# Performance work log

Measured on AMD Instinct MI355X. Metric: run time of the kernel, lower is better.

## Reference

```python
import math
import jax, jax.numpy as jnp
import numpy as np

B, T, C, H = 4, 2048, 1024, 1024

def setup_inputs() -> dict:
    key = jax.random.key(0)
    kx, kk, kq, kv = jax.random.split(key, 4)
    s = 1.0 / math.sqrt(C)
    return {
        "x": jax.random.normal(kx, (B, T, C), dtype=jnp.float32),
        # torch Linear weight is [out, in]; store transposed [in, out] for x @ W
        "Wk": jax.random.uniform(kk, (C, H), dtype=jnp.float32, minval=-s, maxval=s),
        "Wq": jax.random.uniform(kq, (C, H), dtype=jnp.float32, minval=-s, maxval=s),
        "Wv": jax.random.uniform(kv, (C, H), dtype=jnp.float32, minval=-s, maxval=s),
    }

def reference(x, Wk, Wq, Wv):
    K = x @ Wk  # [B,T,H]
    Q = x @ Wq
    V = x @ Wv
    scale = 1.0 / math.sqrt(K.shape[-1])
    wei = jnp.einsum('bth,bsh->bts', Q, K) * scale  # [B,T,T]
    t = x.shape[1]
    causal = jnp.tril(jnp.ones((t, t), dtype=bool))
    wei = jnp.where(causal, wei, -jnp.inf)
    wei = jax.nn.softmax(wei, axis=-1)
    wei = jax.nn.relu(wei)  # no-op mathematically but kept for fidelity
    return jnp.einsum('bts,bsh->bth', wei, V)
```

## Files before the change

### kernel.cpp

```cpp
#include <hip/hip_runtime.h>

typedef _Float16 f16;
typedef _Float16 f16x8 __attribute__((ext_vector_type(8)));
typedef float    f32x4 __attribute__((ext_vector_type(4)));

#define AS3 __attribute__((address_space(3)))
#define AS1 __attribute__((address_space(1)))

static __device__ __forceinline__ void gld_lds16(const f16* g, f16* l) {
    __builtin_amdgcn_global_load_lds((const AS1 void*)g, (AS3 void*)l, 16, 0, 0);
}


__global__ void cvt_x(const float* __restrict__ x, f16* __restrict__ xh) {
    int i = blockIdx.x * blockDim.x + threadIdx.x;
    const f32x4* xv = (const f32x4*)x;
    f32x4 a = xv[2 * i], b = xv[2 * i + 1];
    f16x8 h;
    h[0] = (f16)a[0]; h[1] = (f16)a[1]; h[2] = (f16)a[2]; h[3] = (f16)a[3];
    h[4] = (f16)b[0]; h[5] = (f16)b[1]; h[6] = (f16)b[2]; h[7] = (f16)b[3];
    ((f16x8*)xh)[i] = h;
}

__global__ void cvt_transpose_w(const float* __restrict__ Wq, const float* __restrict__ Wk,
                                const float* __restrict__ Wv, f16* __restrict__ Wt) {
    const float* W = blockIdx.z == 0 ? Wq : (blockIdx.z == 1 ? Wk : Wv);
    __shared__ float tile[32][33];
    int tx = threadIdx.x, ty = threadIdx.y;
    int n0 = blockIdx.x * 32, k0 = blockIdx.y * 32;
#pragma unroll
    for (int r = 0; r < 4; ++r)
        tile[ty + r * 8][tx] = W[(size_t)(k0 + ty + r * 8) * 1024 + n0 + tx];
    __syncthreads();
    f16* o = Wt + (size_t)blockIdx.z * 1024 * 1024;
#pragma unroll
    for (int r = 0; r < 4; ++r)
        o[(size_t)(n0 + ty + r * 8) * 1024 + k0 + tx] = (f16)tile[tx][ty + r * 8];
}

template <int MODE>
__global__ __launch_bounds__(256, 4)
void gemm128(const f16* __restrict__ A, int lda, long aStride,
             const f16* __restrict__ B, int ldb, long bStride,
             void* __restrict__ Cout, int ldc, long cStride,
             int ktiles, float scale, float* __restrict__ lsum,
             const f16* __restrict__ A2, const f16* __restrict__ B2,
             void* __restrict__ C2) {
    int bm, bn, bz = blockIdx.z;
    int m0, n0;
    const f16 *Ab, *Bb;
    char* Cb;

    if (MODE == 0) {
        bn = blockIdx.x; bm = blockIdx.y;
        n0 = bn * 128;
        if (bm < 64) {
            m0 = bm * 128;
            Ab = A; Bb = B; Cb = (char*)Cout;
        } else {
            int t = bm - 64;
            int bb = t >> 3;
            m0 = (t & 7) * 128;
            Ab = A2;
            Bb = B2 + (long)bb * 2048 * 1024;
            Cb = (char*)C2 + (long)bb * 1024 * 2048 * sizeof(f16);
        }
    } else if (MODE == 1) {
        int i = blockIdx.x;
        float ff = sqrtf(8.f * (float)i + 1.f);
        bm = (int)((ff - 1.f) * 0.5f);
        while ((bm + 1) * (bm + 2) / 2 <= i) ++bm;
        while (bm * (bm + 1) / 2 > i) --bm;
        bn = i - bm * (bm + 1) / 2;
        m0 = bm * 128; n0 = bn * 128;
        Ab = A + (long)bz * aStride;
        Bb = B + (long)bz * bStride;
        Cb = (char*)Cout + (long)bz * cStride * sizeof(f16);
    } else {
        bn = blockIdx.x; bm = gridDim.y - 1 - blockIdx.y;
        int lim = 4 * (bm + 1); if (lim < ktiles) ktiles = lim;
        m0 = bm * 128; n0 = bn * 128;
        Ab = A + (long)bz * aStride;
        Bb = B + (long)bz * bStride;
        Cb = (char*)Cout + (long)bz * cStride * sizeof(float);
    }

    __shared__ f16 lds[2 * 8192];

    const int tid = threadIdx.x;
    const int wave = tid >> 6, lane = tid & 63;
    const int q = lane >> 4, rr = lane & 15;
    const int wm = (wave >> 1) * 64, wn = (wave & 1) * 64;

    const int kcs = (((tid & 3) - (lane >> 4)) & 3) * 8;
    const f16* pA = Ab + (long)(m0 + (tid >> 2)) * lda + kcs;
    const f16* pB = Bb + (long)(n0 + (tid >> 2)) * ldb + kcs;

    auto stage = [&](int kt, int buf) {
        const int k0 = kt * 32;
        f16* lA = lds + buf * 8192 + wave * 512;
        f16* lB = lds + buf * 8192 + 4096 + wave * 512;
#pragma unroll
        for (int it = 0; it < 2; ++it) {
            gld_lds16(pA + (long)it * 64 * lda + k0, lA + it * 2048);
            gld_lds16(pB + (long)it * 64 * ldb + k0, lB + it * 2048);
        }
    };

    const int slotf = ((q + (rr >> 2)) & 3) * 8;

    f32x4 acc[4][4] = {};

    stage(0, 0);
    __syncthreads();

    for (int kt = 0; kt < ktiles; ++kt) {
        const int cur = kt & 1;
        if (kt + 1 < ktiles) stage(kt + 1, 1 - cur);
        const f16* bufA = lds + cur * 8192;
        const f16* bufB = bufA + 4096;
        f16x8 af[4], bf[4];
#pragma unroll
        for (int i = 0; i < 4; ++i)
            af[i] = *(const f16x8*)&bufA[(wm + i * 16 + rr) * 32 + slotf];
#pragma unroll
        for (int j = 0; j < 4; ++j)
            bf[j] = *(const f16x8*)&bufB[(wn + j * 16 + rr) * 32 + slotf];
#pragma unroll
        for (int i = 0; i < 4; ++i)
#pragma unroll
            for (int j = 0; j < 4; ++j)
                acc[i][j] = __builtin_amdgcn_mfma_f32_16x16x32_f16(af[i], bf[j], acc[i][j], 0, 0, 0);
        __syncthreads();
    }

#pragma unroll
    for (int i = 0; i < 4; ++i) {
#pragma unroll
        for (int r2 = 0; r2 < 4; ++r2) {
            const int row = wm + i * 16 + q * 4 + r2;
            float psum = 0.f;
            float inv = 1.f;
            if (MODE == 2) inv = 1.0f / lsum[bz * 2048 + m0 + row];
#pragma unroll
            for (int j = 0; j < 4; ++j) {
                const int col = wn + j * 16 + rr;
                float v = acc[i][j][r2] * scale;
                long idx = (long)(m0 + row) * ldc + n0 + col;
                if (MODE == 1) {
                    v = __expf(v);
                    if (n0 + col > m0 + row) v = 0.f;
                    psum += v;
                    ((f16*)Cb)[idx] = (f16)v;
                } else if (MODE == 0) {
                    ((f16*)Cb)[idx] = (f16)v;
                } else {
                    ((float*)Cb)[idx] = v * inv;
                }
            }
            if (MODE == 1) {
                psum += __shfl_xor(psum, 1, 64);
                psum += __shfl_xor(psum, 2, 64);
                psum += __shfl_xor(psum, 4, 64);
                psum += __shfl_xor(psum, 8, 64);
                if (rr == 0) atomicAdd(&lsum[bz * 2048 + m0 + row], psum);
            }
        }
    }
}

extern "C" void kernel_launch(void* const* d_in, const int* in_sizes, int n_in,
                              void* d_out, int out_size, void* d_ws, size_t ws_size,
                              hipStream_t stream) {
    (void)in_sizes; (void)n_in; (void)out_size; (void)ws_size;
    const float* x  = (const float*)d_in[0];
    const float* Wk = (const float*)d_in[1];
    const float* Wq = (const float*)d_in[2];
    const float* Wv = (const float*)d_in[3];
    float* out = (float*)d_out;

    const long MB = 1l << 20;
    char* ws = (char*)d_ws;
    f16*   qk   = (f16*)(ws);
    f16*   Vt   = (f16*)(ws + 32 * MB);
    f16*   P    = (f16*)(ws + 48 * MB);
    float* lsum = (float*)(ws + 80 * MB);
    f16*   xh   = (f16*)(ws + 81 * MB);
    f16*   Wt   = (f16*)(ws + 97 * MB);

    cvt_x<<<4096, 256, 0, stream>>>(x, xh);
    cvt_transpose_w<<<dim3(32, 32, 3), dim3(32, 8), 0, stream>>>(Wq, Wk, Wv, Wt);
    hipMemsetAsync(lsum, 0, 4 * 2048 * sizeof(float), stream);

    gemm128<0><<<dim3(16, 96, 1), 256, 0, stream>>>(xh, 1024, 0, Wt, 1024, 0,
                                                    qk, 2048, 0, 32, 1.0f, nullptr,
                                                    Wt + 2l * 1024 * 1024, xh, Vt);
    gemm128<1><<<dim3(136, 1, 4), 256, 0, stream>>>(qk, 2048, 2048l * 2048,
                                                    qk + 1024, 2048, 2048l * 2048,
                                                    P, 2048, 2048l * 2048, 32, 0.03125f, lsum,
                                                    nullptr, nullptr, nullptr);
    gemm128<2><<<dim3(8, 16, 4), 256, 0, stream>>>(P, 2048, 2048l * 2048,
                                                   Vt, 2048, 1024l * 2048,
                                                   out, 1024, 2048l * 1024, 64, 1.0f, lsum,
                                                   nullptr, nullptr, nullptr);
}
```

Measured before the change: 246.4 us.

## Fuse conversion kernels, add 2-wave projection GEMM, widen epilogue stores

Merges the x conversion, weight transpose and lsum memset into one launch, which removes two launches and a memset. The projection GEMM becomes a new 128-thread kernel in which each wave computes a 128x64 tile, giving more register reuse per wave at lower occupancy. The epilogues of all GEMMs pair adjacent columns with a lane shuffle so each store writes 32 or 64 bits instead of 16 or 32. The risks are register pressure from the larger accumulator array and fewer waves available to hide latency.

```diff
diff --git a/kernel.cpp b/kernel.cpp
--- a/kernel.cpp
+++ b/kernel.cpp
@@ -11,31 +11,131 @@
     __builtin_amdgcn_global_load_lds((const AS1 void*)g, (AS3 void*)l, 16, 0, 0);
 }
 
-
-__global__ void cvt_x(const float* __restrict__ x, f16* __restrict__ xh) {
-    int i = blockIdx.x * blockDim.x + threadIdx.x;
-    const f32x4* xv = (const f32x4*)x;
-    f32x4 a = xv[2 * i], b = xv[2 * i + 1];
-    f16x8 h;
-    h[0] = (f16)a[0]; h[1] = (f16)a[1]; h[2] = (f16)a[2]; h[3] = (f16)a[3];
-    h[4] = (f16)b[0]; h[5] = (f16)b[1]; h[6] = (f16)b[2]; h[7] = (f16)b[3];
-    ((f16x8*)xh)[i] = h;
-}
-
-__global__ void cvt_transpose_w(const float* __restrict__ Wq, const float* __restrict__ Wk,
-                                const float* __restrict__ Wv, f16* __restrict__ Wt) {
-    const float* W = blockIdx.z == 0 ? Wq : (blockIdx.z == 1 ? Wk : Wv);
+static __device__ __forceinline__ unsigned pack_f16(float a, float b) {
+    union { f16 h[2]; unsigned u; } p;
+    p.h[0] = (f16)a; p.h[1] = (f16)b;
+    return p.u;
+}
+
+__global__ void cvt_fused(const float* __restrict__ x, f16* __restrict__ xh,
+                          const float* __restrict__ Wq, const float* __restrict__ Wk,
+                          const float* __restrict__ Wv, f16* __restrict__ Wt,
+                          float* __restrict__ lsum) {
     __shared__ float tile[32][33];
-    int tx = threadIdx.x, ty = threadIdx.y;
-    int n0 = blockIdx.x * 32, k0 = blockIdx.y * 32;
-#pragma unroll
-    for (int r = 0; r < 4; ++r)
-        tile[ty + r * 8][tx] = W[(size_t)(k0 + ty + r * 8) * 1024 + n0 + tx];
+    const int bid = blockIdx.x;
+    if (bid < 4096) {
+        int i = bid * 256 + threadIdx.x;
+        const f32x4* xv = (const f32x4*)x;
+        f32x4 a = xv[2 * i], b = xv[2 * i + 1];
+        f16x8 h;
+        h[0] = (f16)a[0]; h[1] = (f16)a[1]; h[2] = (f16)a[2]; h[3] = (f16)a[3];
+        h[4] = (f16)b[0]; h[5] = (f16)b[1]; h[6] = (f16)b[2]; h[7] = (f16)b[3];
+        ((f16x8*)xh)[i] = h;
+        if (bid == 0) {
+#pragma unroll
+            for (int k = 0; k < 32; ++k) lsum[threadIdx.x * 32 + k] = 0.f;
+        }
+    } else {
+        int b2 = bid - 4096;
+        int bx = b2 & 31, by = (b2 >> 5) & 31, bz = b2 >> 10;
+        const float* W = bz == 0 ? Wq : (bz == 1 ? Wk : Wv);
+        int tx = threadIdx.x & 31, ty = threadIdx.x >> 5;
+        int n0 = bx * 32, k0 = by * 32;
+#pragma unroll
+        for (int r = 0; r < 4; ++r)
+            tile[ty + r * 8][tx] = W[(size_t)(k0 + ty + r * 8) * 1024 + n0 + tx];
+        __syncthreads();
+        f16* o = Wt + (size_t)bz * 1024 * 1024;
+#pragma unroll
+        for (int r = 0; r < 4; ++r)
+            o[(size_t)(n0 + ty + r * 8) * 1024 + k0 + tx] = (f16)tile[tx][ty + r * 8];
+    }
+}
+
+__global__ __launch_bounds__(128, 2)
+void gemmw2(const f16* __restrict__ A, const f16* __restrict__ B, f16* __restrict__ C,
+            const f16* __restrict__ A2, const f16* __restrict__ B2, f16* __restrict__ C2) {
+    const int bn = blockIdx.x, bm = blockIdx.y;
+    const int n0 = bn * 128;
+    int m0; const f16 *Ab, *Bb; f16* Cb;
+    if (bm < 64) {
+        m0 = bm * 128; Ab = A; Bb = B; Cb = C;
+    } else {
+        int t = bm - 64, bb = t >> 3;
+        m0 = (t & 7) * 128;
+        Ab = A2;
+        Bb = B2 + (long)bb * 2048 * 1024;
+        Cb = C2 + (long)bb * 1024 * 2048;
+    }
+    const int lda = 1024, ldb = 1024, ldc = 2048, ktiles = 32;
+
+    __shared__ f16 lds[2 * 8192];
+
+    const int tid = threadIdx.x;
+    const int wave = tid >> 6, lane = tid & 63;
+    const int q = lane >> 4, rr = lane & 15;
+    const int wn = wave * 64;
+
+    const int kcs = (((lane & 3) - (lane >> 4)) & 3) * 8;
+    const f16* pA = Ab + (long)(m0 + (tid >> 2)) * lda + kcs;
+    const f16* pB = Bb + (long)(n0 + (tid >> 2)) * ldb + kcs;
+
+    auto stage = [&](int kt, int buf) {
+        const int k0 = kt * 32;
+        f16* base = lds + buf * 8192 + wave * 512;
+#pragma unroll
+        for (int it = 0; it < 4; ++it) {
+            gld_lds16(pA + (long)it * 32 * lda + k0, base + it * 1024);
+            gld_lds16(pB + (long)it * 32 * ldb + k0, base + 4096 + it * 1024);
+        }
+    };
+
+    const int slotf = ((q + (rr >> 2)) & 3) * 8;
+
+    f32x4 acc[8][4] = {};
+
+    stage(0, 0);
     __syncthreads();
-    f16* o = Wt + (size_t)blockIdx.z * 1024 * 1024;
-#pragma unroll
-    for (int r = 0; r < 4; ++r)
-        o[(size_t)(n0 + ty + r * 8) * 1024 + k0 + tx] = (f16)tile[tx][ty + r * 8];
+
+    for (int kt = 0; kt < ktiles; ++kt) {
+        const int cur = kt & 1;
+        if (kt + 1 < ktiles) stage(kt + 1, 1 - cur);
+        const f16* bufA = lds + cur * 8192;
+        const f16* bufB = bufA + 4096;
+        f16x8 bf[4];
+#pragma unroll
+        for (int j = 0; j < 4; ++j)
+            bf[j] = *(const f16x8*)&bufB[(wn + j * 16 + rr) * 32 + slotf];
+#pragma unroll
+        for (int ih = 0; ih < 2; ++ih) {
+            f16x8 af[4];
+#pragma unroll
+            for (int i = 0; i < 4; ++i)
+                af[i] = *(const f16x8*)&bufA[((ih * 4 + i) * 16 + rr) * 32 + slotf];
+#pragma unroll
+            for (int i = 0; i < 4; ++i)
+#pragma unroll
+                for (int j = 0; j < 4; ++j)
+                    acc[ih * 4 + i][j] =
+                        __builtin_amdgcn_mfma_f32_16x16x32_f16(af[i], bf[j], acc[ih * 4 + i][j], 0, 0, 0);
+        }
+        __syncthreads();
+    }
+
+#pragma unroll
+    for (int i = 0; i < 8; ++i)
+#pragma unroll
+        for (int r2 = 0; r2 < 4; ++r2) {
+            const int row = i * 16 + q * 4 + r2;
+#pragma unroll
+            for (int j = 0; j < 4; ++j) {
+                const int col = wn + j * 16 + rr;
+                float v = acc[i][j][r2];
+                float vo = __shfl_xor(v, 1, 64);
+                if ((rr & 1) == 0)
+                    *(unsigned*)(Cb + (long)(m0 + row) * ldc + n0 + col) = pack_f16(v, vo);
+            }
+        }
 }
 
 template <int MODE>
@@ -43,29 +143,13 @@
 void gemm128(const f16* __restrict__ A, int lda, long aStride,
              const f16* __restrict__ B, int ldb, long bStride,
              void* __restrict__ Cout, int ldc, long cStride,
-             int ktiles, float scale, float* __restrict__ lsum,
-             const f16* __restrict__ A2, const f16* __restrict__ B2,
-             void* __restrict__ C2) {
+             int ktiles, float scale, float* __restrict__ lsum) {
     int bm, bn, bz = blockIdx.z;
     int m0, n0;
     const f16 *Ab, *Bb;
     char* Cb;
 
-    if (MODE == 0) {
-        bn = blockIdx.x; bm = blockIdx.y;
-        n0 = bn * 128;
-        if (bm < 64) {
-            m0 = bm * 128;
-            Ab = A; Bb = B; Cb = (char*)Cout;
-        } else {
-            int t = bm - 64;
-            int bb = t >> 3;
-            m0 = (t & 7) * 128;
-            Ab = A2;
-            Bb = B2 + (long)bb * 2048 * 1024;
-            Cb = (char*)C2 + (long)bb * 1024 * 2048 * sizeof(f16);
-        }
-    } else if (MODE == 1) {
+    if (MODE == 1) {
         int i = blockIdx.x;
         float ff = sqrtf(8.f * (float)i + 1.f);
         bm = (int)((ff - 1.f) * 0.5f);
@@ -151,11 +235,14 @@
                     v = __expf(v);
                     if (n0 + col > m0 + row) v = 0.f;
                     psum += v;
-                    ((f16*)Cb)[idx] = (f16)v;
-                } else if (MODE == 0) {
-                    ((f16*)Cb)[idx] = (f16)v;
+                    float vo = __shfl_xor(v, 1, 64);
+                    if ((rr & 1) == 0)
+                        *(unsigned*)((f16*)Cb + idx) = pack_f16(v, vo);
                 } else {
-                    ((float*)Cb)[idx] = v * inv;
+                    v *= inv;
+                    float vo = __shfl_xor(v, 1, 64);
+                    if ((rr & 1) == 0)
+                        *(float2*)((float*)Cb + idx) = make_float2(v, vo);
                 }
             }
             if (MODE == 1) {
@@ -188,19 +275,14 @@
     f16*   xh   = (f16*)(ws + 81 * MB);
     f16*   Wt   = (f16*)(ws + 97 * MB);
 
-    cvt_x<<<4096, 256, 0, stream>>>(x, xh);
-    cvt_transpose_w<<<dim3(32, 32, 3), dim3(32, 8), 0, stream>>>(Wq, Wk, Wv, Wt);
-    hipMemsetAsync(lsum, 0, 4 * 2048 * sizeof(float), stream);
-
-    gemm128<0><<<dim3(16, 96, 1), 256, 0, stream>>>(xh, 1024, 0, Wt, 1024, 0,
-                                                    qk, 2048, 0, 32, 1.0f, nullptr,
-                                                    Wt + 2l * 1024 * 1024, xh, Vt);
+    cvt_fused<<<7168, 256, 0, stream>>>(x, xh, Wq, Wk, Wv, Wt, lsum);
+
+    gemmw2<<<dim3(16, 96), 128, 0, stream>>>(xh, Wt, qk,
+                                             Wt + 2l * 1024 * 1024, xh, Vt);
     gemm128<1><<<dim3(136, 1, 4), 256, 0, stream>>>(qk, 2048, 2048l * 2048,
                                                     qk + 1024, 2048, 2048l * 2048,
-                                                    P, 2048, 2048l * 2048, 32, 0.03125f, lsum,
-                                                    nullptr, nullptr, nullptr);
+                                                    P, 2048, 2048l * 2048, 32, 0.03125f, lsum);
     gemm128<2><<<dim3(8, 16, 4), 256, 0, stream>>>(P, 2048, 2048l * 2048,
                                                    Vt, 2048, 1024l * 2048,
-                                                   out, 1024, 2048l * 1024, 64, 1.0f, lsum,
-                                                   nullptr, nullptr, nullptr);
-}
+                                                   out, 1024, 2048l * 1024, 64, 1.0f, lsum);
+}
```

Result: slower. 255.9 us (+3.9%).

## Compute softmax row sums via MFMA in PV gemm, fuse convert kernels, pack stores

Applied to the files above, without the earlier changes.

Drops the atomicAdd row-sum reduction and the lsum memset. In the P·V gemm, waves with wn==0 accumulate row sums of P with an extra MFMA against a ones vector and share them through LDS. The two fp32->fp16 conversion kernels are merged into one launch. Epilogue stores are paired across lanes with a shuffle so each store writes two elements. The cost is extra MFMA work on half the waves, an extra barrier, and row sums taken from the fp16-rounded P values.

```diff
diff --git a/kernel.cpp b/kernel.cpp
--- a/kernel.cpp
+++ b/kernel.cpp
@@ -11,31 +11,40 @@
     __builtin_amdgcn_global_load_lds((const AS1 void*)g, (AS3 void*)l, 16, 0, 0);
 }
 
-
-__global__ void cvt_x(const float* __restrict__ x, f16* __restrict__ xh) {
-    int i = blockIdx.x * blockDim.x + threadIdx.x;
-    const f32x4* xv = (const f32x4*)x;
-    f32x4 a = xv[2 * i], b = xv[2 * i + 1];
-    f16x8 h;
-    h[0] = (f16)a[0]; h[1] = (f16)a[1]; h[2] = (f16)a[2]; h[3] = (f16)a[3];
-    h[4] = (f16)b[0]; h[5] = (f16)b[1]; h[6] = (f16)b[2]; h[7] = (f16)b[3];
-    ((f16x8*)xh)[i] = h;
-}
-
-__global__ void cvt_transpose_w(const float* __restrict__ Wq, const float* __restrict__ Wk,
-                                const float* __restrict__ Wv, f16* __restrict__ Wt) {
-    const float* W = blockIdx.z == 0 ? Wq : (blockIdx.z == 1 ? Wk : Wv);
+static __device__ __forceinline__ unsigned pack_f16(float a, float b) {
+    union { f16 h[2]; unsigned u; } p;
+    p.h[0] = (f16)a; p.h[1] = (f16)b;
+    return p.u;
+}
+
+__global__ void cvt_fused(const float* __restrict__ x, f16* __restrict__ xh,
+                          const float* __restrict__ Wq, const float* __restrict__ Wk,
+                          const float* __restrict__ Wv, f16* __restrict__ Wt) {
     __shared__ float tile[32][33];
-    int tx = threadIdx.x, ty = threadIdx.y;
-    int n0 = blockIdx.x * 32, k0 = blockIdx.y * 32;
-#pragma unroll
-    for (int r = 0; r < 4; ++r)
-        tile[ty + r * 8][tx] = W[(size_t)(k0 + ty + r * 8) * 1024 + n0 + tx];
-    __syncthreads();
-    f16* o = Wt + (size_t)blockIdx.z * 1024 * 1024;
-#pragma unroll
-    for (int r = 0; r < 4; ++r)
-        o[(size_t)(n0 + ty + r * 8) * 1024 + k0 + tx] = (f16)tile[tx][ty + r * 8];
+    const int bid = blockIdx.x;
+    if (bid < 4096) {
+        int i = bid * 256 + threadIdx.x;
+        const f32x4* xv = (const f32x4*)x;
+        f32x4 a = xv[2 * i], b = xv[2 * i + 1];
+        f16x8 h;
+        h[0] = (f16)a[0]; h[1] = (f16)a[1]; h[2] = (f16)a[2]; h[3] = (f16)a[3];
+        h[4] = (f16)b[0]; h[5] = (f16)b[1]; h[6] = (f16)b[2]; h[7] = (f16)b[3];
+        ((f16x8*)xh)[i] = h;
+    } else {
+        int b2 = bid - 4096;
+        int bx = b2 & 31, by = (b2 >> 5) & 31, bz = b2 >> 10;
+        const float* W = bz == 0 ? Wq : (bz == 1 ? Wk : Wv);
+        int tx = threadIdx.x & 31, ty = threadIdx.x >> 5;
+        int n0 = bx * 32, k0 = by * 32;
+#pragma unroll
+        for (int r = 0; r < 4; ++r)
+            tile[ty + r * 8][tx] = W[(size_t)(k0 + ty + r * 8) * 1024 + n0 + tx];
+        __syncthreads();
+        f16* o = Wt + (size_t)bz * 1024 * 1024;
+#pragma unroll
+        for (int r = 0; r < 4; ++r)
+            o[(size_t)(n0 + ty + r * 8) * 1024 + k0 + tx] = (f16)tile[tx][ty + r * 8];
+    }
 }
 
 template <int MODE>
@@ -43,7 +52,7 @@
 void gemm128(const f16* __restrict__ A, int lda, long aStride,
              const f16* __restrict__ B, int ldb, long bStride,
              void* __restrict__ Cout, int ldc, long cStride,
-             int ktiles, float scale, float* __restrict__ lsum,
+             int ktiles, float scale,
              const f16* __restrict__ A2, const f16* __restrict__ B2,
              void* __restrict__ C2) {
     int bm, bn, bz = blockIdx.z;
@@ -110,6 +119,13 @@
     const int slotf = ((q + (rr >> 2)) & 3) * 8;
 
     f32x4 acc[4][4] = {};
+    f32x4 accs[4] = {};
+    f16x8 onef;
+    const bool sumwave = (MODE == 2) && (wn == 0);
+    if (MODE == 2) {
+#pragma unroll
+        for (int t = 0; t < 8; ++t) onef[t] = (f16)1.0f;
+    }
 
     stage(0, 0);
     __syncthreads();
@@ -127,11 +143,32 @@
         for (int j = 0; j < 4; ++j)
             bf[j] = *(const f16x8*)&bufB[(wn + j * 16 + rr) * 32 + slotf];
 #pragma unroll
-        for (int i = 0; i < 4; ++i)
+        for (int i = 0; i < 4; ++i) {
 #pragma unroll
             for (int j = 0; j < 4; ++j)
                 acc[i][j] = __builtin_amdgcn_mfma_f32_16x16x32_f16(af[i], bf[j], acc[i][j], 0, 0, 0);
+            if (sumwave)
+                accs[i] = __builtin_amdgcn_mfma_f32_16x16x32_f16(af[i], onef, accs[i], 0, 0, 0);
+        }
         __syncthreads();
+    }
+
+    float invr[4][4];
+    if (MODE == 2) {
+        float* rs = (float*)lds;
+        if (sumwave && rr == 0) {
+#pragma unroll
+            for (int i = 0; i < 4; ++i)
+#pragma unroll
+                for (int r2 = 0; r2 < 4; ++r2)
+                    rs[wm + i * 16 + q * 4 + r2] = accs[i][r2];
+        }
+        __syncthreads();
+#pragma unroll
+        for (int i = 0; i < 4; ++i)
+#pragma unroll
+            for (int r2 = 0; r2 < 4; ++r2)
+                invr[i][r2] = 1.0f / rs[wm + i * 16 + q * 4 + r2];
     }
 
 #pragma unroll
@@ -139,9 +176,6 @@
 #pragma unroll
         for (int r2 = 0; r2 < 4; ++r2) {
             const int row = wm + i * 16 + q * 4 + r2;
-            float psum = 0.f;
-            float inv = 1.f;
-            if (MODE == 2) inv = 1.0f / lsum[bz * 2048 + m0 + row];
 #pragma unroll
             for (int j = 0; j < 4; ++j) {
                 const int col = wn + j * 16 + rr;
@@ -150,20 +184,19 @@
                 if (MODE == 1) {
                     v = __expf(v);
                     if (n0 + col > m0 + row) v = 0.f;
-                    psum += v;
-                    ((f16*)Cb)[idx] = (f16)v;
+                    float vo = __shfl_xor(v, 1, 64);
+                    if ((rr & 1) == 0)
+                        *(unsigned*)((f16*)Cb + idx) = pack_f16(v, vo);
                 } else if (MODE == 0) {
-                    ((f16*)Cb)[idx] = (f16)v;
+                    float vo = __shfl_xor(v, 1, 64);
+                    if ((rr & 1) == 0)
+                        *(unsigned*)((f16*)Cb + idx) = pack_f16(v, vo);
                 } else {
-                    ((float*)Cb)[idx] = v * inv;
+                    v *= invr[i][r2];
+                    float vo = __shfl_xor(v, 1, 64);
+                    if ((rr & 1) == 0)
+                        *(float2*)((float*)Cb + idx) = make_float2(v, vo);
                 }
-            }
-            if (MODE == 1) {
-                psum += __shfl_xor(psum, 1, 64);
-                psum += __shfl_xor(psum, 2, 64);
-                psum += __shfl_xor(psum, 4, 64);
-                psum += __shfl_xor(psum, 8, 64);
-                if (rr == 0) atomicAdd(&lsum[bz * 2048 + m0 + row], psum);
             }
         }
     }
@@ -184,23 +217,20 @@
     f16*   qk   = (f16*)(ws);
     f16*   Vt   = (f16*)(ws + 32 * MB);
     f16*   P    = (f16*)(ws + 48 * MB);
-    float* lsum = (float*)(ws + 80 * MB);
     f16*   xh   = (f16*)(ws + 81 * MB);
     f16*   Wt   = (f16*)(ws + 97 * MB);
 
-    cvt_x<<<4096, 256, 0, stream>>>(x, xh);
-    cvt_transpose_w<<<dim3(32, 32, 3), dim3(32, 8), 0, stream>>>(Wq, Wk, Wv, Wt);
-    hipMemsetAsync(lsum, 0, 4 * 2048 * sizeof(float), stream);
+    cvt_fused<<<7168, 256, 0, stream>>>(x, xh, Wq, Wk, Wv, Wt);
 
     gemm128<0><<<dim3(16, 96, 1), 256, 0, stream>>>(xh, 1024, 0, Wt, 1024, 0,
-                                                    qk, 2048, 0, 32, 1.0f, nullptr,
+                                                    qk, 2048, 0, 32, 1.0f,
                                                     Wt + 2l * 1024 * 1024, xh, Vt);
     gemm128<1><<<dim3(136, 1, 4), 256, 0, stream>>>(qk, 2048, 2048l * 2048,
                                                     qk + 1024, 2048, 2048l * 2048,
-                                                    P, 2048, 2048l * 2048, 32, 0.03125f, lsum,
+                                                    P, 2048, 2048l * 2048, 32, 0.03125f,
                                                     nullptr, nullptr, nullptr);
     gemm128<2><<<dim3(8, 16, 4), 256, 0, stream>>>(P, 2048, 2048l * 2048,
                                                    Vt, 2048, 1024l * 2048,
-                                                   out, 1024, 2048l * 1024, 64, 1.0f, lsum,
+                                                   out, 1024, 2048l * 1024, 64, 1.0f,
                                                    nullptr, nullptr, nullptr);
 }
```

Result: slower. 255.9 us (+3.9%).
